# Kernel tuning notes

Hardware: AMD Instinct MI355X
Metric: run time of the kernel (lower is better)

The kernel has to match this reference:

```python
import jax, jax.numpy as jnp
import numpy as np

MODEL = 2048
LATENT = 512
POS = 1024
NH = 16
HD = MODEL // NH        # 128
PHD = POS // NH         # 64
THETA = 50000.0


def _rope_tables(S, dim, base=THETA):
    inv_freq = 1.0 / (base ** (jnp.arange(0, dim, 2, dtype=jnp.float32) / dim))
    t = jnp.arange(S, dtype=jnp.float32)
    freqs = jnp.outer(t, inv_freq)                  # [S, dim/2]
    emb = jnp.concatenate([freqs, freqs], axis=-1)  # [S, dim]
    return jnp.cos(emb), jnp.sin(emb)


def _rotate_half(x):
    h = x.shape[-1] // 2
    return jnp.concatenate([-x[..., h:], x[..., :h]], axis=-1)


def _apply_rope(x, cos, sin):
    # x: [..., S, dim]; cos/sin: [S, dim]
    return x * cos + _rotate_half(x) * sin


def setup_inputs() -> dict:
    key = jax.random.key(0)
    ks = jax.random.split(key, 16)
    std = 0.02
    d = {
        'x':      jax.random.normal(ks[0], (2, 2048, MODEL), jnp.float32),
        'w_qkv':  jax.random.normal(ks[1], (MODEL, 3 * LATENT), jnp.float32) * std,
        'b_qkv':  jnp.zeros((3 * LATENT,), jnp.float32),
        'w_qup':  jax.random.normal(ks[2], (LATENT, MODEL), jnp.float32) * std,
        'b_qup':  jnp.zeros((MODEL,), jnp.float32),
        'w_kup':  jax.random.normal(ks[3], (LATENT, MODEL), jnp.float32) * std,
        'b_kup':  jnp.zeros((MODEL,), jnp.float32),
        'w_vup':  jax.random.normal(ks[4], (LATENT, MODEL), jnp.float32) * std,
        'b_vup':  jnp.zeros((MODEL,), jnp.float32),
        'w_qpos': jax.random.normal(ks[5], (LATENT, POS), jnp.float32) * std,
        'b_qpos': jnp.zeros((POS,), jnp.float32),
        'w_kpos': jax.random.normal(ks[6], (MODEL, PHD), jnp.float32) * std,
        'b_kpos': jnp.zeros((PHD,), jnp.float32),
        'w_o':    jax.random.normal(ks[7], (MODEL, MODEL), jnp.float32) * std,
        'b_o':    jnp.zeros((MODEL,), jnp.float32),
    }
    return d


def reference(x, w_qkv, b_qkv, w_qup, b_qup, w_kup, b_kup, w_vup, b_vup,
              w_qpos, b_qpos, w_kpos, b_kpos, w_o, b_o):
    B, S, _ = x.shape
    # fused down-projection into shared latent
    latent_qkv = x @ w_qkv + b_qkv                       # [B,S,3L]
    lq, lk, lv = jnp.split(latent_qkv, 3, axis=-1)       # each [B,S,L]

    cos, sin = _rope_tables(S, PHD)

    # decoupled positional key (shared across heads), RoPE on sub-slice
    pos_k = x @ w_kpos + b_kpos                          # [B,S,PHD]
    pos_k = _apply_rope(pos_k, cos, sin)

    # up-projections
    q = (lq @ w_qup + b_qup).reshape(B, S, NH, HD).transpose(0, 2, 1, 3)
    k = (lk @ w_kup + b_kup).reshape(B, S, NH, HD).transpose(0, 2, 1, 3)
    v = (lv @ w_vup + b_vup).reshape(B, S, NH, HD).transpose(0, 2, 1, 3)

    pos_q = (lq @ w_qpos + b_qpos).reshape(B, S, NH, PHD).transpose(0, 2, 1, 3)
    pos_q = _apply_rope(pos_q, cos, sin)                 # [B,NH,S,PHD]

    pos_kh = jnp.broadcast_to(pos_k[:, None], (B, NH, S, PHD))
    q = jnp.concatenate([q, pos_q], axis=-1)             # [B,NH,S,HD+PHD]
    k = jnp.concatenate([k, pos_kh], axis=-1)

    scale = 1.0 / jnp.sqrt(jnp.asarray(HD + PHD, x.dtype))
    scores = jnp.einsum('bhqd,bhkd->bhqk', q, k) * scale
    causal = jnp.tril(jnp.ones((S, S), bool))
    scores = jnp.where(causal, scores, jnp.finfo(scores.dtype).min)
    p = jax.nn.softmax(scores, axis=-1)
    attn = jnp.einsum('bhqk,bhkd->bhqd', p, v)           # [B,NH,S,HD]
    attn = attn.transpose(0, 2, 1, 3).reshape(B, S, MODEL)
    return attn @ w_o + b_o
```

## Files before the change

kernel.cpp:

```cpp
#include <hip/hip_runtime.h>
#include <cstdint>
#include <cstddef>

typedef __bf16 bf16x8 __attribute__((ext_vector_type(8)));
typedef float  f32x4  __attribute__((ext_vector_type(4)));
typedef unsigned short us8 __attribute__((ext_vector_type(8)));
typedef unsigned short us4 __attribute__((ext_vector_type(4)));

__device__ __forceinline__ unsigned short f2bf(float f) {
  union { float f; unsigned u; } v; v.f = f;
  unsigned r = v.u + 0x7FFFu + ((v.u >> 16) & 1u);
  return (unsigned short)(r >> 16);
}
__device__ __forceinline__ float b2f(unsigned short h) {
  union { unsigned u; float f; } v; v.u = ((unsigned)h) << 16;
  return v.f;
}
__device__ __forceinline__ f32x4 mfma16(bf16x8 a, bf16x8 b, f32x4 c) {
  return __builtin_amdgcn_mfma_f32_16x16x32_bf16(a, b, c, 0, 0, 0);
}
__device__ __forceinline__ void gl_lds16(const unsigned short* g, unsigned short* l) {
  __builtin_amdgcn_global_load_lds(
      (const __attribute__((address_space(1))) void*)g,
      (__attribute__((address_space(3))) void*)l, 16, 0, 0);
}

__global__ void prep_misc_kernel(const float* __restrict__ b_qkv,
                                 const float* __restrict__ b_kpos,
                                 const float* __restrict__ b_qup,
                                 const float* __restrict__ b_qpos,
                                 float* __restrict__ bias1,
                                 float* __restrict__ bias2q,
                                 float* __restrict__ costab,
                                 float* __restrict__ sintab,
                                 unsigned short* __restrict__ wB1pad) {
  int i = blockIdx.x * 256 + threadIdx.x;
  if (i < 65536) {
    int s = i >> 5, f = i & 31;
    float inv = powf(50000.0f, -(float)f / 32.0f);
    float a = (float)s * inv;
    costab[i] = cosf(a);
    sintab[i] = sinf(a);
  }
  if (i < 1664) bias1[i] = (i < 1536) ? b_qkv[i] : (i < 1600 ? b_kpos[i - 1536] : 0.0f);
  if (i < 3072) bias2q[i] = (i < 2048) ? b_qup[i] : b_qpos[i - 2048];
  if (i < 131072) wB1pad[i] = 0;
}

__global__ void convx_kernel(const float* __restrict__ in,
                             unsigned short* __restrict__ out, int n4) {
  int i = blockIdx.x * 256 + threadIdx.x;
  if (i < n4) {
    float4 v = ((const float4*)in)[i];
    us4 o;
    o[0] = f2bf(v.x); o[1] = f2bf(v.y); o[2] = f2bf(v.z); o[3] = f2bf(v.w);
    ((us4*)out)[i] = o;
  }
}

__global__ void tconv_kernel(const float* __restrict__ in, int ldin,
                             unsigned short* __restrict__ out, int ldo) {
  __shared__ float tile[32][33];
  int c0 = blockIdx.x * 32, r0 = blockIdx.y * 32;
  int tx = threadIdx.x & 31, ty = threadIdx.x >> 5;
  for (int j = 0; j < 4; ++j)
    tile[ty + j * 8][tx] = in[(size_t)(r0 + ty + j * 8) * ldin + c0 + tx];
  __syncthreads();
  for (int j = 0; j < 4; ++j)
    out[(size_t)(c0 + ty + j * 8) * ldo + r0 + tx] = f2bf(tile[tx][ty + j * 8]);
}

template <int OUT_MODE>
__global__ __launch_bounds__(256, 2)
void gemm_bt_kernel(const unsigned short* __restrict__ A, int lda,
                    const unsigned short* __restrict__ Bt, int ldb,
                    void* __restrict__ Cout, int ldc,
                    const float* __restrict__ bias, int K) {
  __shared__ unsigned short smem[32768];
  int tid = threadIdx.x;
  int wave = tid >> 6, lane = tid & 63;
  int g = lane >> 4, r = lane & 15;
  int wr = wave >> 1, wc = wave & 1;
  long brow = (long)blockIdx.y * 128, bcol = (long)blockIdx.x * 128;

  int srowl = lane >> 3;
  int sw = ((lane & 7) ^ (srowl & 7)) * 8;
  const unsigned short* Abase = A + (brow + wave * 32 + srowl) * (long)lda + sw;
  const unsigned short* Bbase = Bt + (bcol + wave * 32 + srowl) * (long)ldb + sw;

  f32x4 acc[4][4];
  for (int mi = 0; mi < 4; ++mi)
    for (int ni = 0; ni < 4; ++ni)
      acc[mi][ni] = f32x4{0.f, 0.f, 0.f, 0.f};

  auto stage = [&](int buf, int k0) {
    unsigned short* ab = smem + buf * 16384;
    unsigned short* bb = ab + 8192;
    for (int c = 0; c < 4; ++c) {
      gl_lds16(Abase + (size_t)c * 8 * lda + k0, ab + (wave * 32 + c * 8) * 64);
      gl_lds16(Bbase + (size_t)c * 8 * ldb + k0, bb + (wave * 32 + c * 8) * 64);
    }
  };

  int rx = (r & 7) << 4;
  int nt = K >> 6;

  stage(0, 0);
  for (int t = 0; t < nt; ++t) {
    if (t + 1 < nt) {
      stage((t + 1) & 1, (t + 1) << 6);
      asm volatile("s_waitcnt vmcnt(8)" ::: "memory");
    } else {
      asm volatile("s_waitcnt vmcnt(0)" ::: "memory");
    }
    __builtin_amdgcn_sched_barrier(0);
    __builtin_amdgcn_s_barrier();
    __builtin_amdgcn_sched_barrier(0);
    const char* Ab = (const char*)(smem + (t & 1) * 16384);
    const char* Bb = Ab + 16384;
    for (int kk = 0; kk < 2; ++kk) {
      bf16x8 af[4], bfv[4];
      for (int mi = 0; mi < 4; ++mi)
        af[mi] = *(const bf16x8*)(Ab + (size_t)(wr * 64 + mi * 16 + r) * 128 +
                                  ((kk * 64 + g * 16) ^ rx));
      for (int ni = 0; ni < 4; ++ni)
        bfv[ni] = *(const bf16x8*)(Bb + (size_t)(wc * 64 + ni * 16 + r) * 128 +
                                   ((kk * 64 + g * 16) ^ rx));
      for (int mi = 0; mi < 4; ++mi)
        for (int ni = 0; ni < 4; ++ni)
          acc[mi][ni] = mfma16(af[mi], bfv[ni], acc[mi][ni]);
    }
    __builtin_amdgcn_sched_barrier(0);
    __builtin_amdgcn_s_barrier();
  }

  if (OUT_MODE == 2) {
    for (int mi = 0; mi < 4; ++mi)
      for (int ni = 0; ni < 4; ++ni) {
        int col = wc * 64 + ni * 16 + r;
        float bv = bias[bcol + col];
        int rowb = wr * 64 + mi * 16 + g * 4;
        for (int i = 0; i < 4; ++i)
          smem[col * 136 + rowb + i] = f2bf(acc[mi][ni][i] + bv);
      }
    __syncthreads();
    int col = tid >> 1, half = tid & 1;
    int bh = (int)(brow >> 11) * 16 + (int)(bcol >> 7);
    unsigned short* outp = (unsigned short*)Cout +
                           ((size_t)bh * 128 + col) * 2048 + (brow & 2047);
    for (int j = 0; j < 8; ++j) {
      int row0 = half * 64 + j * 8;
      *(us8*)(outp + row0) = *(const us8*)&smem[col * 136 + row0];
    }
    return;
  }

  for (int mi = 0; mi < 4; ++mi)
    for (int ni = 0; ni < 4; ++ni) {
      long col = bcol + wc * 64 + ni * 16 + r;
      float bv = bias ? bias[col] : 0.0f;
      long rowb = brow + wr * 64 + mi * 16 + g * 4;
      for (int i = 0; i < 4; ++i) {
        float v = acc[mi][ni][i] + bv;
        if (OUT_MODE == 1)
          ((float*)Cout)[(rowb + i) * (long)ldc + col] = v;
        else
          ((unsigned short*)Cout)[(rowb + i) * (long)ldc + col] = f2bf(v);
      }
    }
}

__global__ void rope_kernel(const unsigned short* __restrict__ tmp_q,
                            const unsigned short* __restrict__ latext,
                            const float* __restrict__ costab,
                            const float* __restrict__ sintab,
                            unsigned short* __restrict__ posqr,
                            unsigned short* __restrict__ poskr) {
  int idx = blockIdx.x * 256 + threadIdx.x;
  const unsigned short* src;
  unsigned short* dst;
  int s, dp0;
  if (idx < 524288) {
    int rowA = idx >> 7, rem = idx & 127;
    int h = rem >> 3;
    dp0 = (rem & 7) * 8;
    s = rowA & 2047;
    src = tmp_q + (size_t)rowA * 3072 + 2048 + h * 64;
    dst = posqr + (size_t)rowA * 1024 + h * 64 + dp0;
  } else if (idx < 557056) {
    int j = idx - 524288;
    int rowA = j >> 3;
    dp0 = (j & 7) * 8;
    s = rowA & 2047;
    src = latext + (size_t)rowA * 1664 + 1536;
    dst = poskr + (size_t)rowA * 64 + dp0;
  } else {
    return;
  }
  us8 x1 = *(const us8*)(src + dp0);
  us8 x2 = *(const us8*)(src + (dp0 ^ 32));
  int f0 = dp0 & 31;
  const float* cp = costab + s * 32 + f0;
  const float* sp = sintab + s * 32 + f0;
  bool low = dp0 < 32;
  us8 o;
  for (int e = 0; e < 8; ++e) {
    float a = b2f(x1[e]), b = b2f(x2[e]);
    float v = low ? (a * cp[e] - b * sp[e]) : (a * cp[e] + b * sp[e]);
    o[e] = f2bf(v);
  }
  *(us8*)dst = o;
}

__device__ __forceinline__ void task_decode(int t, int& qt, int& seg, int& bh) {
  if (t < 1024) {
    qt = 31 - (t >> 7); int rem = t & 127; seg = rem >> 5; bh = rem & 31;
  } else if (t < 1792) {
    int t2 = t - 1024; int qi = t2 / 96; int rem = t2 - qi * 96;
    qt = 23 - qi; seg = rem >> 5; bh = rem & 31;
  } else if (t < 2304) {
    int t3 = t - 1792; qt = 15 - (t3 >> 6); int rem = t3 & 63; seg = rem >> 5; bh = rem & 31;
  } else {
    int t4 = t - 2304; qt = 7 - (t4 >> 5); seg = 0; bh = t4 & 31;
  }
}
__device__ __forceinline__ int task_slot(int qt, int seg, int bh) {
  if (qt >= 24) return (31 - qt) * 128 + seg * 32 + bh;
  if (qt >= 16) return 1024 + (23 - qt) * 96 + seg * 32 + bh;
  return 1792 + (15 - qt) * 64 + seg * 32 + bh;
}

__global__ __launch_bounds__(256, 2)
void flash_kernel(const unsigned short* __restrict__ tmp_q,
                  const unsigned short* __restrict__ tmp_k,
                  const unsigned short* __restrict__ posqr,
                  const unsigned short* __restrict__ poskr,
                  const unsigned short* __restrict__ vT,
                  unsigned short* __restrict__ ob,
                  unsigned short* __restrict__ Opart,
                  float* __restrict__ mlbuf,
                  int* __restrict__ counter) {
  const int S = 2048;
  int tid = threadIdx.x, wave = tid >> 6, lane = tid & 63;
  int g = lane >> 4, r = lane & 15;
  const float sl2 = 1.44269504f / 13.8564064605510183f;
  const float DEFER = 96.0f;

  __shared__ unsigned short Klds[32 * 192];
  __shared__ unsigned short Vlds[128 * 32];
  __shared__ unsigned short Plds[4][16][40];
  __shared__ int s_tile;
  char* Kb = (char*)Klds;
  char* Vb = (char*)Vlds;
  int rx7 = (r & 7) << 4, rx3 = (r & 3) << 4;

  us8 onesu;
  for (int e = 0; e < 8; ++e) onesu[e] = 0x3F80;
  bf16x8 ones = *(const bf16x8*)&onesu;

  int kn_row[2], kn_seg[2];
  for (int j = 0; j < 2; ++j) {
    int slot = j * 256 + tid;
    kn_row[j] = slot >> 4;
    kn_seg[j] = slot & 15;
  }
  int kr_row = tid >> 3, kr_seg = tid & 7;
  int v_row[2], v_seg[2];
  for (int j = 0; j < 2; ++j) {
    int slot = j * 256 + tid;
    v_row[j] = slot >> 2;
    v_seg[j] = slot & 3;
  }

  for (;;) {
    if (tid == 0) s_tile = atomicAdd(counter, 1);
    __syncthreads();
    int t = s_tile;
    if (t >= 2560) return;
    int qt, seg, bh;
    task_decode(t, qt, seg, bh);
    int b = bh >> 4, h = bh & 15;
    int qbase = qt * 64;
    int cbeg = seg * 16;
    int cend = min(cbeg + 16, 2 * (qt + 1));
    size_t rb = (size_t)b * 2048;

    const unsigned short* kpn = tmp_k + rb * 2048 + h * 128;
    const unsigned short* kpr = poskr + rb * 64;
    const unsigned short* vp = vT + (size_t)bh * 128 * S;

    bf16x8 qf[6];
    {
      size_t qrowA = rb + qbase + wave * 16 + r;
      const unsigned short* qn = tmp_q + qrowA * 3072 + h * 128 + g * 8;
      for (int c = 0; c < 4; ++c) qf[c] = *(const bf16x8*)(qn + c * 32);
      const unsigned short* qr_ = posqr + qrowA * 1024 + h * 64 + g * 8;
      qf[4] = *(const bf16x8*)(qr_);
      qf[5] = *(const bf16x8*)(qr_ + 32);
    }

    f32x4 acc[8];
    for (int d = 0; d < 8; ++d) acc[d] = f32x4{0.f, 0.f, 0.f, 0.f};
    f32x4 lacc = {0.f, 0.f, 0.f, 0.f};
    float m_r[4];
    for (int i = 0; i < 4; ++i) m_r[i] = -3.0e38f;

    us8 kreg[2], krope, vreg[2];
    {
      int kv0 = cbeg * 32;
      for (int j = 0; j < 2; ++j)
        kreg[j] = *(const us8*)(kpn + (size_t)(kv0 + kn_row[j]) * 2048 + kn_seg[j] * 8);
      krope = *(const us8*)(kpr + (size_t)(kv0 + kr_row) * 64 + kr_seg * 8);
      for (int j = 0; j < 2; ++j)
        vreg[j] = *(const us8*)(vp + (size_t)v_row[j] * S + kv0 + v_seg[j] * 8);
    }

    for (int ch = cbeg; ch < cend; ++ch) {
      for (int j = 0; j < 2; ++j)
        *(us8*)(Kb + (size_t)kn_row[j] * 384 +
                ((kn_seg[j] ^ (kn_row[j] & 7)) << 4)) = kreg[j];
      *(us8*)(Kb + (size_t)kr_row * 384 +
              (((16 + kr_seg) ^ (kr_row & 7)) << 4)) = krope;
      for (int j = 0; j < 2; ++j)
        *(us8*)(Vb + (size_t)v_row[j] * 64 +
                ((v_seg[j] ^ (v_row[j] & 3)) << 4)) = vreg[j];
      asm volatile("s_waitcnt lgkmcnt(0)" ::: "memory");
      __builtin_amdgcn_sched_barrier(0);
      __builtin_amdgcn_s_barrier();
      __builtin_amdgcn_sched_barrier(0);
      if (ch + 1 < cend) {
        int kv1 = (ch + 1) * 32;
        for (int j = 0; j < 2; ++j)
          kreg[j] = *(const us8*)(kpn + (size_t)(kv1 + kn_row[j]) * 2048 + kn_seg[j] * 8);
        krope = *(const us8*)(kpr + (size_t)(kv1 + kr_row) * 64 + kr_seg * 8);
        for (int j = 0; j < 2; ++j)
          vreg[j] = *(const us8*)(vp + (size_t)v_row[j] * S + kv1 + v_seg[j] * 8);
      }
      int kv0 = ch * 32;

      f32x4 sc0 = {0.f, 0.f, 0.f, 0.f}, sc1 = {0.f, 0.f, 0.f, 0.f};
      __builtin_amdgcn_s_setprio(1);
      for (int c = 0; c < 6; ++c) {
        bf16x8 kf0 = *(const bf16x8*)(Kb + (size_t)r * 384 + (((c * 4 + g) << 4) ^ rx7));
        sc0 = mfma16(qf[c], kf0, sc0);
      }
      for (int c = 0; c < 6; ++c) {
        bf16x8 kf1 = *(const bf16x8*)(Kb + (size_t)(16 + r) * 384 + (((c * 4 + g) << 4) ^ rx7));
        sc1 = mfma16(qf[c], kf1, sc1);
      }
      __builtin_amdgcn_s_setprio(0);

      int kj0 = kv0 + r, kj1 = kv0 + 16 + r;
      int qi0 = qbase + wave * 16 + g * 4;
      for (int i = 0; i < 4; ++i) {
        if (kj0 > qi0 + i) sc0[i] = -1e30f;
        if (kj1 > qi0 + i) sc1[i] = -1e30f;
      }

      float tl[4];
      bool ok = true;
      for (int i = 0; i < 4; ++i) {
        tl[i] = fmaxf(sc0[i], sc1[i]);
        ok = ok && (tl[i] - m_r[i] <= DEFER);
      }
      if (!__all(ok)) {
        for (int i = 0; i < 4; ++i) {
          float tm = tl[i];
          for (int off = 1; off < 16; off <<= 1) tm = fmaxf(tm, __shfl_xor(tm, off, 64));
          float mnew = fmaxf(m_r[i], tm);
          float corr = exp2f((m_r[i] - mnew) * sl2);
          lacc[i] *= corr;
          for (int d = 0; d < 8; ++d) acc[d][i] *= corr;
          m_r[i] = mnew;
        }
      }
      float p0[4], p1[4];
      for (int i = 0; i < 4; ++i) {
        p0[i] = exp2f((sc0[i] - m_r[i]) * sl2);
        p1[i] = exp2f((sc1[i] - m_r[i]) * sl2);
      }

      for (int i = 0; i < 4; ++i) {
        Plds[wave][g * 4 + i][r] = f2bf(p0[i]);
        Plds[wave][g * 4 + i][16 + r] = f2bf(p1[i]);
      }
      bf16x8 pa = *(const bf16x8*)&Plds[wave][r][g * 8];
      __builtin_amdgcn_s_setprio(1);
      lacc = mfma16(pa, ones, lacc);
      for (int dt = 0; dt < 8; ++dt) {
        bf16x8 vf = *(const bf16x8*)(Vb + (size_t)(dt * 16 + r) * 64 + ((g << 4) ^ rx3));
        acc[dt] = mfma16(pa, vf, acc[dt]);
      }
      __builtin_amdgcn_s_setprio(0);
      __builtin_amdgcn_sched_barrier(0);
      __builtin_amdgcn_s_barrier();
    }

    if (qt <= 7) {
      for (int i = 0; i < 4; ++i) {
        float inv = 1.0f / lacc[i];
        int row = qbase + wave * 16 + g * 4 + i;
        size_t base = (rb + row) * 2048 + h * 128;
        for (int dt = 0; dt < 8; ++dt)
          ob[base + dt * 16 + r] = f2bf(acc[dt][i] * inv);
      }
    } else {
      unsigned short* op = Opart + (size_t)t * 8192;
      for (int i = 0; i < 4; ++i) {
        int row = wave * 16 + g * 4 + i;
        for (int dt = 0; dt < 8; ++dt)
          op[row * 128 + dt * 16 + r] = f2bf(acc[dt][i]);
        if (r == 0) {
          mlbuf[(size_t)t * 128 + row * 2]     = m_r[i];
          mlbuf[(size_t)t * 128 + row * 2 + 1] = lacc[i];
        }
      }
    }
  }
}

__global__ void merge_kernel(const unsigned short* __restrict__ Opart,
                             const float* __restrict__ mlbuf,
                             unsigned short* __restrict__ ob) {
  int qt = 8 + (blockIdx.x >> 5), bh = blockIdx.x & 31;
  int b = bh >> 4, h = bh & 15;
  int tid = threadIdx.x;
  int row = tid >> 2, c0 = (tid & 3) * 32;
  const float sl2 = 1.44269504f / 13.8564064605510183f;
  int ns = (qt >= 24) ? 4 : (qt >= 16 ? 3 : 2);

  size_t slot[4];
  float m[4], l[4], w[4];
  float M = -3.0e38f;
#pragma unroll
  for (int j = 0; j < 4; ++j) {
    if (j < ns) {
      slot[j] = task_slot(qt, j, bh);
      m[j] = mlbuf[slot[j] * 128 + row * 2];
      l[j] = mlbuf[slot[j] * 128 + row * 2 + 1];
      M = fmaxf(M, m[j]);
    }
  }
  float L = 0.f;
#pragma unroll
  for (int j = 0; j < 4; ++j)
    if (j < ns) { w[j] = exp2f((m[j] - M) * sl2); L += w[j] * l[j]; }
  float invL = 1.f / L;
#pragma unroll
  for (int j = 0; j < 4; ++j) if (j < ns) w[j] *= invL;

  float o[32];
#pragma unroll
  for (int e = 0; e < 32; ++e) o[e] = 0.f;
#pragma unroll
  for (int j = 0; j < 4; ++j) {
    if (j < ns) {
      const unsigned short* pp = Opart + slot[j] * 8192 + row * 128 + c0;
      for (int blk = 0; blk < 4; ++blk) {
        us8 v = *(const us8*)(pp + blk * 8);
        for (int e = 0; e < 8; ++e) o[blk * 8 + e] += w[j] * b2f(v[e]);
      }
    }
  }
  size_t obase = ((size_t)b * 2048 + qt * 64 + row) * 2048 + h * 128 + c0;
  for (int blk = 0; blk < 4; ++blk) {
    us8 st;
    for (int e = 0; e < 8; ++e) st[e] = f2bf(o[blk * 8 + e]);
    *(us8*)(ob + obase + blk * 8) = st;
  }
}

extern "C" void kernel_launch(void* const* d_in, const int* in_sizes, int n_in,
                              void* d_out, int out_size, void* d_ws, size_t ws_size,
                              hipStream_t stream) {
  const float* x      = (const float*)d_in[0];
  const float* w_qkv  = (const float*)d_in[1];
  const float* b_qkv  = (const float*)d_in[2];
  const float* w_qup  = (const float*)d_in[3];
  const float* b_qup  = (const float*)d_in[4];
  const float* w_kup  = (const float*)d_in[5];
  const float* b_kup  = (const float*)d_in[6];
  const float* w_vup  = (const float*)d_in[7];
  const float* b_vup  = (const float*)d_in[8];
  const float* w_qpos = (const float*)d_in[9];
  const float* b_qpos = (const float*)d_in[10];
  const float* w_kpos = (const float*)d_in[11];
  const float* b_kpos = (const float*)d_in[12];
  const float* w_o    = (const float*)d_in[13];
  const float* b_o    = (const float*)d_in[14];
  (void)in_sizes; (void)n_in; (void)out_size; (void)ws_size;

  char* ws = (char*)d_ws;
  size_t off = 0;
  auto alloc = [&](size_t bytes) -> char* {
    char* p = ws + off;
    off += (bytes + 255) & ~(size_t)255;
    return p;
  };

  unsigned short* xb     = (unsigned short*)alloc(16777216);
  unsigned short* wB1    = (unsigned short*)alloc(6815744);
  unsigned short* wB2q   = (unsigned short*)alloc(3145728);
  unsigned short* wB2k   = (unsigned short*)alloc(2097152);
  unsigned short* wB2v   = (unsigned short*)alloc(2097152);
  unsigned short* wBo    = (unsigned short*)alloc(8388608);
  float*          bias1  = (float*)alloc(1664 * 4);
  float*          bias2q = (float*)alloc(3072 * 4);
  float*          costab = (float*)alloc(262144);
  float*          sintab = (float*)alloc(262144);
  unsigned short* latext = (unsigned short*)alloc(13631488);
  unsigned short* tmp_q  = (unsigned short*)alloc(25165824);
  unsigned short* tmp_k  = (unsigned short*)alloc(16777216);
  unsigned short* vTbuf  = (unsigned short*)alloc(16777216);
  unsigned short* posqr  = (unsigned short*)alloc(8388608);
  unsigned short* poskr  = (unsigned short*)alloc(524288);
  unsigned short* Opart  = (unsigned short*)alloc(41943040);
  float*          mlbuf  = (float*)alloc(1310720);
  int*            counter= (int*)alloc(256);
  unsigned short* attnb  = xb;

  prep_misc_kernel<<<512, 256, 0, stream>>>(b_qkv, b_kpos, b_qup, b_qpos,
                                            bias1, bias2q, costab, sintab,
                                            wB1 + (size_t)1600 * 2048);
  convx_kernel<<<8192, 256, 0, stream>>>(x, xb, 2097152);
  tconv_kernel<<<dim3(48, 64), 256, 0, stream>>>(w_qkv, 1536, wB1, 2048);
  tconv_kernel<<<dim3(2, 64), 256, 0, stream>>>(w_kpos, 64, wB1 + (size_t)1536 * 2048, 2048);
  tconv_kernel<<<dim3(64, 16), 256, 0, stream>>>(w_qup, 2048, wB2q, 512);
  tconv_kernel<<<dim3(32, 16), 256, 0, stream>>>(w_qpos, 1024, wB2q + (size_t)2048 * 512, 512);
  tconv_kernel<<<dim3(64, 16), 256, 0, stream>>>(w_kup, 2048, wB2k, 512);
  tconv_kernel<<<dim3(64, 16), 256, 0, stream>>>(w_vup, 2048, wB2v, 512);
  tconv_kernel<<<dim3(64, 64), 256, 0, stream>>>(w_o, 2048, wBo, 2048);

  gemm_bt_kernel<0><<<dim3(13, 32), 256, 0, stream>>>(xb, 2048, wB1, 2048,
                                                      latext, 1664, bias1, 2048);
  gemm_bt_kernel<0><<<dim3(24, 32), 256, 0, stream>>>(latext, 1664, wB2q, 512,
                                                      tmp_q, 3072, bias2q, 512);
  gemm_bt_kernel<0><<<dim3(16, 32), 256, 0, stream>>>(latext + 512, 1664, wB2k, 512,
                                                      tmp_k, 2048, b_kup, 512);
  gemm_bt_kernel<2><<<dim3(16, 32), 256, 0, stream>>>(latext + 1024, 1664, wB2v, 512,
                                                      vTbuf, 2048, b_vup, 512);
  rope_kernel<<<2176, 256, 0, stream>>>(tmp_q, latext, costab, sintab, posqr, poskr);
  hipMemsetAsync(counter, 0, 4, stream);
  flash_kernel<<<1024, 256, 0, stream>>>(tmp_q, tmp_k, posqr, poskr, vTbuf,
                                         attnb, Opart, mlbuf, counter);
  merge_kernel<<<768, 256, 0, stream>>>(Opart, mlbuf, attnb);
  gemm_bt_kernel<1><<<dim3(16, 32), 256, 0, stream>>>(attnb, 2048, wBo, 2048,
                                                      d_out, 2048, b_o, 2048);
}
```

Before: 295.9 us.

## Deepen GEMM pipeline to 4 stages with K=32 tiles, skip masking, enlarge flash grid

The GEMM now stages K in 32-wide tiles through a 4-deep LDS ring instead of a 64-wide double buffer, with a new swizzle and staged waitcnt levels. The goal is to keep more global loads in flight and hide memory latency. The flash kernel skips the causal-mask loop for fully unmasked chunks, and its launch grid grows from 1024 to 1280 blocks. The grid change assumes the kernel's work distribution tolerates the extra blocks, and the new swizzle/read mapping risks LDS bank conflicts or indexing errors.

After: 311.8 us. 5.4% more time.

```diff
diff --git a/kernel.cpp b/kernel.cpp
--- a/kernel.cpp
+++ b/kernel.cpp
@@ -83,10 +83,12 @@
   int wr = wave >> 1, wc = wave & 1;
   long brow = (long)blockIdx.y * 128, bcol = (long)blockIdx.x * 128;
 
-  int srowl = lane >> 3;
-  int sw = ((lane & 7) ^ (srowl & 7)) * 8;
-  const unsigned short* Abase = A + (brow + wave * 32 + srowl) * (long)lda + sw;
-  const unsigned short* Bbase = Bt + (bcol + wave * 32 + srowl) * (long)ldb + sw;
+  int Rl = lane >> 3, blkl = lane & 7;
+  int blkp = blkl ^ Rl;
+  int grow = 2 * Rl + (blkp >> 2);
+  int scol = (blkp & 3) * 8;
+  const unsigned short* Abase = A + (brow + wave * 32 + grow) * (long)lda + scol;
+  const unsigned short* Bbase = Bt + (bcol + wave * 32 + grow) * (long)ldb + scol;
 
   f32x4 acc[4][4];
   for (int mi = 0; mi < 4; ++mi)
@@ -94,47 +96,49 @@
       acc[mi][ni] = f32x4{0.f, 0.f, 0.f, 0.f};
 
   auto stage = [&](int buf, int k0) {
-    unsigned short* ab = smem + buf * 16384;
-    unsigned short* bb = ab + 8192;
-    for (int c = 0; c < 4; ++c) {
-      gl_lds16(Abase + (size_t)c * 8 * lda + k0, ab + (wave * 32 + c * 8) * 64);
-      gl_lds16(Bbase + (size_t)c * 8 * ldb + k0, bb + (wave * 32 + c * 8) * 64);
+    unsigned short* ab = smem + buf * 8192;
+    unsigned short* bb = ab + 4096;
+    for (int c = 0; c < 2; ++c) {
+      gl_lds16(Abase + (size_t)c * 16 * lda + k0, ab + (wave * 16 + c * 8) * 64);
+      gl_lds16(Bbase + (size_t)c * 16 * ldb + k0, bb + (wave * 16 + c * 8) * 64);
     }
   };
 
-  int rx = (r & 7) << 4;
-  int nt = K >> 6;
-
-  stage(0, 0);
+  int rhalf = r >> 1;
+  int rx = ((((r & 1) << 2) | g) ^ rhalf) << 4;
+  int nt = K >> 5;
+
+  stage(0, 0); stage(1, 32); stage(2, 64);
   for (int t = 0; t < nt; ++t) {
-    if (t + 1 < nt) {
-      stage((t + 1) & 1, (t + 1) << 6);
+    if (t + 3 < nt) {
+      stage((t + 3) & 3, (t + 3) << 5);
+      asm volatile("s_waitcnt vmcnt(12)" ::: "memory");
+    } else if (t + 2 < nt) {
       asm volatile("s_waitcnt vmcnt(8)" ::: "memory");
+    } else if (t + 1 < nt) {
+      asm volatile("s_waitcnt vmcnt(4)" ::: "memory");
     } else {
       asm volatile("s_waitcnt vmcnt(0)" ::: "memory");
     }
     __builtin_amdgcn_sched_barrier(0);
     __builtin_amdgcn_s_barrier();
     __builtin_amdgcn_sched_barrier(0);
-    const char* Ab = (const char*)(smem + (t & 1) * 16384);
-    const char* Bb = Ab + 16384;
-    for (int kk = 0; kk < 2; ++kk) {
-      bf16x8 af[4], bfv[4];
-      for (int mi = 0; mi < 4; ++mi)
-        af[mi] = *(const bf16x8*)(Ab + (size_t)(wr * 64 + mi * 16 + r) * 128 +
-                                  ((kk * 64 + g * 16) ^ rx));
+    const char* Ab = (const char*)(smem + (t & 3) * 8192);
+    const char* Bb = Ab + 8192;
+    bf16x8 af[4], bfv[4];
+    for (int mi = 0; mi < 4; ++mi)
+      af[mi] = *(const bf16x8*)(Ab + (size_t)(wr * 32 + mi * 8 + rhalf) * 128 + rx);
+    for (int ni = 0; ni < 4; ++ni)
+      bfv[ni] = *(const bf16x8*)(Bb + (size_t)(wc * 32 + ni * 8 + rhalf) * 128 + rx);
+    for (int mi = 0; mi < 4; ++mi)
       for (int ni = 0; ni < 4; ++ni)
-        bfv[ni] = *(const bf16x8*)(Bb + (size_t)(wc * 64 + ni * 16 + r) * 128 +
-                                   ((kk * 64 + g * 16) ^ rx));
-      for (int mi = 0; mi < 4; ++mi)
-        for (int ni = 0; ni < 4; ++ni)
-          acc[mi][ni] = mfma16(af[mi], bfv[ni], acc[mi][ni]);
-    }
+        acc[mi][ni] = mfma16(af[mi], bfv[ni], acc[mi][ni]);
     __builtin_amdgcn_sched_barrier(0);
     __builtin_amdgcn_s_barrier();
   }
 
   if (OUT_MODE == 2) {
+    __syncthreads();
     for (int mi = 0; mi < 4; ++mi)
       for (int ni = 0; ni < 4; ++ni) {
         int col = wc * 64 + ni * 16 + r;
@@ -350,11 +354,14 @@
       }
       __builtin_amdgcn_s_setprio(0);
 
-      int kj0 = kv0 + r, kj1 = kv0 + 16 + r;
-      int qi0 = qbase + wave * 16 + g * 4;
-      for (int i = 0; i < 4; ++i) {
-        if (kj0 > qi0 + i) sc0[i] = -1e30f;
-        if (kj1 > qi0 + i) sc1[i] = -1e30f;
+      int qi_min = qbase + wave * 16;
+      if (kv0 + 31 > qi_min) {
+        int kj0 = kv0 + r, kj1 = kv0 + 16 + r;
+        int qi0 = qi_min + g * 4;
+        for (int i = 0; i < 4; ++i) {
+          if (kj0 > qi0 + i) sc0[i] = -1e30f;
+          if (kj1 > qi0 + i) sc1[i] = -1e30f;
+        }
       }
 
       float tl[4];
@@ -541,7 +548,7 @@
                                                       vTbuf, 2048, b_vup, 512);
   rope_kernel<<<2176, 256, 0, stream>>>(tmp_q, latext, costab, sintab, posqr, poskr);
   hipMemsetAsync(counter, 0, 4, stream);
-  flash_kernel<<<1024, 256, 0, stream>>>(tmp_q, tmp_k, posqr, poskr, vTbuf,
+  flash_kernel<<<1280, 256, 0, stream>>>(tmp_q, tmp_k, posqr, poskr, vTbuf,
                                          attnb, Opart, mlbuf, counter);
   merge_kernel<<<768, 256, 0, stream>>>(Opart, mlbuf, attnb);
   gemm_bt_kernel<1><<<dim3(16, 32), 256, 0, stream>>>(attnb, 2048, wBo, 2048,
```

## Fuse prep kernels, convert x inside GEMM, merge splits in flash, XCD-swizzle GEMMs

Applied to the files above, without the earlier changes.

Folds all bias, rope-table and weight-transpose kernels into one launch. The first GEMM now loads fp32 x directly and converts it to bf16 in registers, so the separate x conversion pass goes away. Split-KV partials are merged by the last-arriving flash block through an atomic counter, which removes the merge kernel. The change also remaps GEMM block ids across XCDs, skips causal masking on tiles that are fully below the diagonal, and raises flash occupancy to 4 blocks per CU, which tightens register limits and may cause spills.

Measured after the change: 811.7 us. +174.4%, slower.

```diff
diff --git a/kernel.cpp b/kernel.cpp
--- a/kernel.cpp
+++ b/kernel.cpp
@@ -25,49 +25,67 @@
       (__attribute__((address_space(3))) void*)l, 16, 0, 0);
 }
 
-__global__ void prep_misc_kernel(const float* __restrict__ b_qkv,
-                                 const float* __restrict__ b_kpos,
-                                 const float* __restrict__ b_qup,
-                                 const float* __restrict__ b_qpos,
-                                 float* __restrict__ bias1,
-                                 float* __restrict__ bias2q,
-                                 float* __restrict__ costab,
-                                 float* __restrict__ sintab,
-                                 unsigned short* __restrict__ wB1pad) {
-  int i = blockIdx.x * 256 + threadIdx.x;
-  if (i < 65536) {
-    int s = i >> 5, f = i & 31;
-    float inv = powf(50000.0f, -(float)f / 32.0f);
-    float a = (float)s * inv;
-    costab[i] = cosf(a);
-    sintab[i] = sinf(a);
-  }
-  if (i < 1664) bias1[i] = (i < 1536) ? b_qkv[i] : (i < 1600 ? b_kpos[i - 1536] : 0.0f);
-  if (i < 3072) bias2q[i] = (i < 2048) ? b_qup[i] : b_qpos[i - 2048];
-  if (i < 131072) wB1pad[i] = 0;
-}
-
-__global__ void convx_kernel(const float* __restrict__ in,
-                             unsigned short* __restrict__ out, int n4) {
-  int i = blockIdx.x * 256 + threadIdx.x;
-  if (i < n4) {
-    float4 v = ((const float4*)in)[i];
-    us4 o;
-    o[0] = f2bf(v.x); o[1] = f2bf(v.y); o[2] = f2bf(v.z); o[3] = f2bf(v.w);
-    ((us4*)out)[i] = o;
-  }
-}
-
-__global__ void tconv_kernel(const float* __restrict__ in, int ldin,
-                             unsigned short* __restrict__ out, int ldo) {
+__global__ void prep_all_kernel(const float* __restrict__ b_qkv,
+                                const float* __restrict__ b_kpos,
+                                const float* __restrict__ b_qup,
+                                const float* __restrict__ b_qpos,
+                                float* __restrict__ bias1,
+                                float* __restrict__ bias2q,
+                                float* __restrict__ costab,
+                                float* __restrict__ sintab,
+                                unsigned short* __restrict__ wB1,
+                                const float* __restrict__ w_qkv,
+                                const float* __restrict__ w_kpos,
+                                const float* __restrict__ w_qup,
+                                const float* __restrict__ w_qpos,
+                                const float* __restrict__ w_kup,
+                                const float* __restrict__ w_vup,
+                                const float* __restrict__ w_o,
+                                unsigned short* __restrict__ wB2q,
+                                unsigned short* __restrict__ wB2k,
+                                unsigned short* __restrict__ wB2v,
+                                unsigned short* __restrict__ wBo) {
   __shared__ float tile[32][33];
-  int c0 = blockIdx.x * 32, r0 = blockIdx.y * 32;
+  int blk = blockIdx.x;
+  if (blk < 512) {
+    int i = blk * 256 + threadIdx.x;
+    if (i < 65536) {
+      int s = i >> 5, f = i & 31;
+      float inv = powf(50000.0f, -(float)f / 32.0f);
+      float a = (float)s * inv;
+      costab[i] = cosf(a);
+      sintab[i] = sinf(a);
+    }
+    if (i < 1664) bias1[i] = (i < 1536) ? b_qkv[i] : (i < 1600 ? b_kpos[i - 1536] : 0.0f);
+    if (i < 3072) bias2q[i] = (i < 2048) ? b_qup[i] : b_qpos[i - 2048];
+    if (i < 131072) wB1[(size_t)1600 * 2048 + i] = 0;
+    return;
+  }
+  const float* in;
+  unsigned short* out;
+  int ldin, ldo, nx, j;
+  if (blk < 3584)      { j = blk - 512;  in = w_qkv;  ldin = 1536; out = wB1;                        ldo = 2048; nx = 48; }
+  else if (blk < 3712) { j = blk - 3584; in = w_kpos; ldin = 64;   out = wB1 + (size_t)1536 * 2048;  ldo = 2048; nx = 2;  }
+  else if (blk < 4736) { j = blk - 3712; in = w_qup;  ldin = 2048; out = wB2q;                       ldo = 512;  nx = 64; }
+  else if (blk < 5248) { j = blk - 4736; in = w_qpos; ldin = 1024; out = wB2q + (size_t)2048 * 512;  ldo = 512;  nx = 32; }
+  else if (blk < 6272) { j = blk - 5248; in = w_kup;  ldin = 2048; out = wB2k;                       ldo = 512;  nx = 64; }
+  else if (blk < 7296) { j = blk - 6272; in = w_vup;  ldin = 2048; out = wB2v;                       ldo = 512;  nx = 64; }
+  else                 { j = blk - 7296; in = w_o;    ldin = 2048; out = wBo;                        ldo = 2048; nx = 64; }
+  int c0 = (j % nx) * 32, r0 = (j / nx) * 32;
   int tx = threadIdx.x & 31, ty = threadIdx.x >> 5;
-  for (int j = 0; j < 4; ++j)
-    tile[ty + j * 8][tx] = in[(size_t)(r0 + ty + j * 8) * ldin + c0 + tx];
+  for (int jj = 0; jj < 4; ++jj)
+    tile[ty + jj * 8][tx] = in[(size_t)(r0 + ty + jj * 8) * ldin + c0 + tx];
   __syncthreads();
-  for (int j = 0; j < 4; ++j)
-    out[(size_t)(c0 + ty + j * 8) * ldo + r0 + tx] = f2bf(tile[tx][ty + j * 8]);
+  for (int jj = 0; jj < 4; ++jj)
+    out[(size_t)(c0 + ty + jj * 8) * ldo + r0 + tx] = f2bf(tile[tx][ty + jj * 8]);
+}
+
+__device__ __forceinline__ void xcd_decode(int nx, int& bx, int& by) {
+  int bid = blockIdx.x, nwg = gridDim.x;
+  int cpx = nwg >> 3;
+  int wg = (bid & 7) * cpx + (bid >> 3);
+  bx = wg % nx;
+  by = wg / nx;
 }
 
 template <int OUT_MODE>
@@ -75,13 +93,15 @@
 void gemm_bt_kernel(const unsigned short* __restrict__ A, int lda,
                     const unsigned short* __restrict__ Bt, int ldb,
                     void* __restrict__ Cout, int ldc,
-                    const float* __restrict__ bias, int K) {
+                    const float* __restrict__ bias, int K, int nx) {
   __shared__ unsigned short smem[32768];
   int tid = threadIdx.x;
   int wave = tid >> 6, lane = tid & 63;
   int g = lane >> 4, r = lane & 15;
   int wr = wave >> 1, wc = wave & 1;
-  long brow = (long)blockIdx.y * 128, bcol = (long)blockIdx.x * 128;
+  int bx, by;
+  xcd_decode(nx, bx, by);
+  long brow = (long)by * 128, bcol = (long)bx * 128;
 
   int srowl = lane >> 3;
   int sw = ((lane & 7) ^ (srowl & 7)) * 8;
@@ -167,6 +187,96 @@
         else
           ((unsigned short*)Cout)[(rowb + i) * (long)ldc + col] = f2bf(v);
       }
+    }
+}
+
+__global__ __launch_bounds__(256, 2)
+void gemm_a32_kernel(const float* __restrict__ A, int lda,
+                     const unsigned short* __restrict__ Bt, int ldb,
+                     unsigned short* __restrict__ Cout, int ldc,
+                     const float* __restrict__ bias, int K, int nx) {
+  __shared__ unsigned short smem[32768];
+  int tid = threadIdx.x;
+  int wave = tid >> 6, lane = tid & 63;
+  int g = lane >> 4, r = lane & 15;
+  int wr = wave >> 1, wc = wave & 1;
+  int bx, by;
+  xcd_decode(nx, bx, by);
+  long brow = (long)by * 128, bcol = (long)bx * 128;
+
+  int f4c = tid & 15, row0 = tid >> 4;
+  int ablk = f4c >> 1, asub = (f4c & 1) * 8;
+  const float4* Ag = (const float4*)(A + (brow + row0) * (size_t)lda) + f4c;
+
+  int srowl = lane >> 3;
+  int sw = ((lane & 7) ^ (srowl & 7)) * 8;
+  const unsigned short* Bbase = Bt + (bcol + wave * 32 + srowl) * (long)ldb + sw;
+
+  f32x4 acc[4][4];
+  for (int mi = 0; mi < 4; ++mi)
+    for (int ni = 0; ni < 4; ++ni)
+      acc[mi][ni] = f32x4{0.f, 0.f, 0.f, 0.f};
+
+  auto stage_b = [&](int buf, int k0) {
+    unsigned short* bb = smem + 16384 + buf * 8192;
+    for (int c = 0; c < 4; ++c)
+      gl_lds16(Bbase + (size_t)c * 8 * ldb + k0, bb + (wave * 32 + c * 8) * 64);
+  };
+
+  int rx = (r & 7) << 4;
+  int nt = K >> 6;
+
+  float4 areg[8];
+#pragma unroll
+  for (int s = 0; s < 8; ++s) areg[s] = Ag[(size_t)s * 8192];
+  stage_b(0, 0);
+
+  for (int t = 0; t < nt; ++t) {
+    char* alds = (char*)(smem + (t & 1) * 8192);
+#pragma unroll
+    for (int s = 0; s < 8; ++s) {
+      us4 hv;
+      hv[0] = f2bf(areg[s].x); hv[1] = f2bf(areg[s].y);
+      hv[2] = f2bf(areg[s].z); hv[3] = f2bf(areg[s].w);
+      int row = row0 + s * 16;
+      *(us4*)(alds + row * 128 + ((ablk ^ (row & 7)) << 4) + asub) = hv;
+    }
+    asm volatile("s_waitcnt vmcnt(0)" ::: "memory");
+    asm volatile("s_waitcnt lgkmcnt(0)" ::: "memory");
+    __builtin_amdgcn_sched_barrier(0);
+    __builtin_amdgcn_s_barrier();
+    __builtin_amdgcn_sched_barrier(0);
+    if (t + 1 < nt) {
+      int k1 = (t + 1) << 6;
+#pragma unroll
+      for (int s = 0; s < 8; ++s) areg[s] = Ag[(size_t)s * 8192 + (k1 >> 2)];
+      stage_b((t + 1) & 1, k1);
+    }
+    const char* Ab = (const char*)(smem + (t & 1) * 8192);
+    const char* Bb = (const char*)(smem + 16384 + (t & 1) * 8192);
+    for (int kk = 0; kk < 2; ++kk) {
+      bf16x8 af[4], bfv[4];
+      for (int mi = 0; mi < 4; ++mi)
+        af[mi] = *(const bf16x8*)(Ab + (size_t)(wr * 64 + mi * 16 + r) * 128 +
+                                  ((kk * 64 + g * 16) ^ rx));
+      for (int ni = 0; ni < 4; ++ni)
+        bfv[ni] = *(const bf16x8*)(Bb + (size_t)(wc * 64 + ni * 16 + r) * 128 +
+                                   ((kk * 64 + g * 16) ^ rx));
+      for (int mi = 0; mi < 4; ++mi)
+        for (int ni = 0; ni < 4; ++ni)
+          acc[mi][ni] = mfma16(af[mi], bfv[ni], acc[mi][ni]);
+    }
+    __builtin_amdgcn_sched_barrier(0);
+    __builtin_amdgcn_s_barrier();
+  }
+
+  for (int mi = 0; mi < 4; ++mi)
+    for (int ni = 0; ni < 4; ++ni) {
+      long col = bcol + wc * 64 + ni * 16 + r;
+      float bv = bias[col];
+      long rowb = brow + wr * 64 + mi * 16 + g * 4;
+      for (int i = 0; i < 4; ++i)
+        Cout[(rowb + i) * (long)ldc + col] = f2bf(acc[mi][ni][i] + bv);
     }
 }
 
@@ -230,7 +340,7 @@
   return 1792 + (15 - qt) * 64 + seg * 32 + bh;
 }
 
-__global__ __launch_bounds__(256, 2)
+__global__ __launch_bounds__(256, 4)
 void flash_kernel(const unsigned short* __restrict__ tmp_q,
                   const unsigned short* __restrict__ tmp_k,
                   const unsigned short* __restrict__ posqr,
@@ -239,8 +349,10 @@
                   unsigned short* __restrict__ ob,
                   unsigned short* __restrict__ Opart,
                   float* __restrict__ mlbuf,
-                  int* __restrict__ counter) {
+                  int* __restrict__ cbuf) {
   const int S = 2048;
+  int* counter = cbuf;
+  int* done = cbuf + 256;
   int tid = threadIdx.x, wave = tid >> 6, lane = tid & 63;
   int g = lane >> 4, r = lane & 15;
   const float sl2 = 1.44269504f / 13.8564064605510183f;
@@ -249,7 +361,7 @@
   __shared__ unsigned short Klds[32 * 192];
   __shared__ unsigned short Vlds[128 * 32];
   __shared__ unsigned short Plds[4][16][40];
-  __shared__ int s_tile;
+  __shared__ int s_tile, s_done;
   char* Kb = (char*)Klds;
   char* Vb = (char*)Vlds;
   int rx7 = (r & 7) << 4, rx3 = (r & 3) << 4;
@@ -350,11 +462,14 @@
       }
       __builtin_amdgcn_s_setprio(0);
 
-      int kj0 = kv0 + r, kj1 = kv0 + 16 + r;
-      int qi0 = qbase + wave * 16 + g * 4;
-      for (int i = 0; i < 4; ++i) {
-        if (kj0 > qi0 + i) sc0[i] = -1e30f;
-        if (kj1 > qi0 + i) sc1[i] = -1e30f;
+      int qi_min = qbase + wave * 16;
+      if (kv0 + 31 > qi_min) {
+        int kj0 = kv0 + r, kj1 = kv0 + 16 + r;
+        int qi0 = qi_min + g * 4;
+        for (int i = 0; i < 4; ++i) {
+          if (kj0 > qi0 + i) sc0[i] = -1e30f;
+          if (kj1 > qi0 + i) sc1[i] = -1e30f;
+        }
       }
 
       float tl[4];
@@ -415,58 +530,52 @@
           mlbuf[(size_t)t * 128 + row * 2 + 1] = lacc[i];
         }
       }
-    }
-  }
-}
-
-__global__ void merge_kernel(const unsigned short* __restrict__ Opart,
-                             const float* __restrict__ mlbuf,
-                             unsigned short* __restrict__ ob) {
-  int qt = 8 + (blockIdx.x >> 5), bh = blockIdx.x & 31;
-  int b = bh >> 4, h = bh & 15;
-  int tid = threadIdx.x;
-  int row = tid >> 2, c0 = (tid & 3) * 32;
-  const float sl2 = 1.44269504f / 13.8564064605510183f;
-  int ns = (qt >= 24) ? 4 : (qt >= 16 ? 3 : 2);
-
-  size_t slot[4];
-  float m[4], l[4], w[4];
-  float M = -3.0e38f;
-#pragma unroll
-  for (int j = 0; j < 4; ++j) {
-    if (j < ns) {
-      slot[j] = task_slot(qt, j, bh);
-      m[j] = mlbuf[slot[j] * 128 + row * 2];
-      l[j] = mlbuf[slot[j] * 128 + row * 2 + 1];
-      M = fmaxf(M, m[j]);
-    }
-  }
-  float L = 0.f;
-#pragma unroll
-  for (int j = 0; j < 4; ++j)
-    if (j < ns) { w[j] = exp2f((m[j] - M) * sl2); L += w[j] * l[j]; }
-  float invL = 1.f / L;
-#pragma unroll
-  for (int j = 0; j < 4; ++j) if (j < ns) w[j] *= invL;
-
-  float o[32];
-#pragma unroll
-  for (int e = 0; e < 32; ++e) o[e] = 0.f;
-#pragma unroll
-  for (int j = 0; j < 4; ++j) {
-    if (j < ns) {
-      const unsigned short* pp = Opart + slot[j] * 8192 + row * 128 + c0;
-      for (int blk = 0; blk < 4; ++blk) {
-        us8 v = *(const us8*)(pp + blk * 8);
-        for (int e = 0; e < 8; ++e) o[blk * 8 + e] += w[j] * b2f(v[e]);
-      }
-    }
-  }
-  size_t obase = ((size_t)b * 2048 + qt * 64 + row) * 2048 + h * 128 + c0;
-  for (int blk = 0; blk < 4; ++blk) {
-    us8 st;
-    for (int e = 0; e < 8; ++e) st[e] = f2bf(o[blk * 8 + e]);
-    *(us8*)(ob + obase + blk * 8) = st;
+      __threadfence();
+      __syncthreads();
+      int ns = (qt >= 24) ? 4 : (qt >= 16 ? 3 : 2);
+      if (tid == 0) s_done = atomicAdd(&done[(qt - 8) * 32 + bh], 1);
+      __syncthreads();
+      if (s_done == ns - 1) {
+        __threadfence();
+        int row = tid >> 2, c0 = (tid & 3) * 32;
+        float mm[4], ll[4], w[4];
+        float M = -3.0e38f;
+#pragma unroll
+        for (int j = 0; j < 4; ++j) {
+          if (j < ns) {
+            size_t sl = (size_t)task_slot(qt, j, bh);
+            mm[j] = mlbuf[sl * 128 + row * 2];
+            ll[j] = mlbuf[sl * 128 + row * 2 + 1];
+            M = fmaxf(M, mm[j]);
+          }
+        }
+        float L = 0.f;
+#pragma unroll
+        for (int j = 0; j < 4; ++j)
+          if (j < ns) { w[j] = exp2f((mm[j] - M) * sl2); L += w[j] * ll[j]; }
+        float invL = 1.f / L;
+#pragma unroll
+        for (int j = 0; j < 4; ++j) if (j < ns) w[j] *= invL;
+        size_t obase = (rb + qbase + row) * 2048 + h * 128 + c0;
+        for (int blk2 = 0; blk2 < 4; ++blk2) {
+          float o8[8];
+#pragma unroll
+          for (int e = 0; e < 8; ++e) o8[e] = 0.f;
+#pragma unroll
+          for (int j = 0; j < 4; ++j) {
+            if (j < ns) {
+              const unsigned short* pp = Opart + (size_t)task_slot(qt, j, bh) * 8192 +
+                                         row * 128 + c0 + blk2 * 8;
+              us8 v = *(const us8*)pp;
+              for (int e = 0; e < 8; ++e) o8[e] += w[j] * b2f(v[e]);
+            }
+          }
+          us8 st;
+          for (int e = 0; e < 8; ++e) st[e] = f2bf(o8[e]);
+          *(us8*)(ob + obase + blk2 * 8) = st;
+        }
+      }
+    }
   }
 }
 
@@ -498,7 +607,6 @@
     return p;
   };
 
-  unsigned short* xb     = (unsigned short*)alloc(16777216);
   unsigned short* wB1    = (unsigned short*)alloc(6815744);
   unsigned short* wB2q   = (unsigned short*)alloc(3145728);
   unsigned short* wB2k   = (unsigned short*)alloc(2097152);
@@ -516,34 +624,25 @@
   unsigned short* poskr  = (unsigned short*)alloc(524288);
   unsigned short* Opart  = (unsigned short*)alloc(41943040);
   float*          mlbuf  = (float*)alloc(1310720);
-  int*            counter= (int*)alloc(256);
-  unsigned short* attnb  = xb;
-
-  prep_misc_kernel<<<512, 256, 0, stream>>>(b_qkv, b_kpos, b_qup, b_qpos,
-                                            bias1, bias2q, costab, sintab,
-                                            wB1 + (size_t)1600 * 2048);
-  convx_kernel<<<8192, 256, 0, stream>>>(x, xb, 2097152);
-  tconv_kernel<<<dim3(48, 64), 256, 0, stream>>>(w_qkv, 1536, wB1, 2048);
-  tconv_kernel<<<dim3(2, 64), 256, 0, stream>>>(w_kpos, 64, wB1 + (size_t)1536 * 2048, 2048);
-  tconv_kernel<<<dim3(64, 16), 256, 0, stream>>>(w_qup, 2048, wB2q, 512);
-  tconv_kernel<<<dim3(32, 16), 256, 0, stream>>>(w_qpos, 1024, wB2q + (size_t)2048 * 512, 512);
-  tconv_kernel<<<dim3(64, 16), 256, 0, stream>>>(w_kup, 2048, wB2k, 512);
-  tconv_kernel<<<dim3(64, 16), 256, 0, stream>>>(w_vup, 2048, wB2v, 512);
-  tconv_kernel<<<dim3(64, 64), 256, 0, stream>>>(w_o, 2048, wBo, 2048);
-
-  gemm_bt_kernel<0><<<dim3(13, 32), 256, 0, stream>>>(xb, 2048, wB1, 2048,
-                                                      latext, 1664, bias1, 2048);
-  gemm_bt_kernel<0><<<dim3(24, 32), 256, 0, stream>>>(latext, 1664, wB2q, 512,
-                                                      tmp_q, 3072, bias2q, 512);
-  gemm_bt_kernel<0><<<dim3(16, 32), 256, 0, stream>>>(latext + 512, 1664, wB2k, 512,
-                                                      tmp_k, 2048, b_kup, 512);
-  gemm_bt_kernel<2><<<dim3(16, 32), 256, 0, stream>>>(latext + 1024, 1664, wB2v, 512,
-                                                      vTbuf, 2048, b_vup, 512);
+  int*            cbuf   = (int*)alloc(8192);
+  unsigned short* attnb  = (unsigned short*)alloc(16777216);
+
+  prep_all_kernel<<<11392, 256, 0, stream>>>(b_qkv, b_kpos, b_qup, b_qpos,
+                                             bias1, bias2q, costab, sintab, wB1,
+                                             w_qkv, w_kpos, w_qup, w_qpos, w_kup,
+                                             w_vup, w_o, wB2q, wB2k, wB2v, wBo);
+  gemm_a32_kernel<<<416, 256, 0, stream>>>(x, 2048, wB1, 2048,
+                                           latext, 1664, bias1, 2048, 13);
+  gemm_bt_kernel<0><<<768, 256, 0, stream>>>(latext, 1664, wB2q, 512,
+                                             tmp_q, 3072, bias2q, 512, 24);
+  gemm_bt_kernel<0><<<512, 256, 0, stream>>>(latext + 512, 1664, wB2k, 512,
+                                             tmp_k, 2048, b_kup, 512, 16);
+  gemm_bt_kernel<2><<<512, 256, 0, stream>>>(latext + 1024, 1664, wB2v, 512,
+                                             vTbuf, 2048, b_vup, 512, 16);
   rope_kernel<<<2176, 256, 0, stream>>>(tmp_q, latext, costab, sintab, posqr, poskr);
-  hipMemsetAsync(counter, 0, 4, stream);
-  flash_kernel<<<1024, 256, 0, stream>>>(tmp_q, tmp_k, posqr, poskr, vTbuf,
-                                         attnb, Opart, mlbuf, counter);
-  merge_kernel<<<768, 256, 0, stream>>>(Opart, mlbuf, attnb);
-  gemm_bt_kernel<1><<<dim3(16, 32), 256, 0, stream>>>(attnb, 2048, wBo, 2048,
-                                                      d_out, 2048, b_o, 2048);
-}
+  hipMemsetAsync(cbuf, 0, 8192, stream);
+  flash_kernel<<<1280, 256, 0, stream>>>(tmp_q, tmp_k, posqr, poskr, vTbuf,
+                                         attnb, Opart, mlbuf, cbuf);
+  gemm_bt_kernel<1><<<512, 256, 0, stream>>>(attnb, 2048, wBo, 2048,
+                                             d_out, 2048, b_o, 2048, 16);
+}
```
